# Kernel tuning notes

Measured on AMD Instinct MI355X. Metric: run time of the kernel, lower is better.

## Reference

```python
import jax, jax.numpy as jnp
import numpy as np

N_NODES = 100000
N_EDGES = 800000
IN_DIM = 7
HID = 64
HEADS1 = 4
NUM_CLUSTERS = 4
NEG_SLOPE = 0.2


def setup_inputs() -> dict:
    key = jax.random.key(0)
    ks = jax.random.split(key, 24)
    s = 0.1
    inp = {
        "x": jax.random.uniform(ks[0], (N_NODES, IN_DIM), dtype=jnp.float32),
        "edge_index": jax.random.randint(ks[1], (2, N_EDGES), 0, N_NODES, dtype=jnp.int32),
        "edge_attr": jax.random.normal(ks[2], (N_EDGES, 1), dtype=jnp.float32),
        "assignments": jax.random.randint(ks[3], (N_NODES,), 0, NUM_CLUSTERS, dtype=jnp.int32),
        "W1": jax.random.normal(ks[4], (IN_DIM, HEADS1 * HID), dtype=jnp.float32) * s,
        "att_src1": jax.random.normal(ks[5], (HEADS1, HID), dtype=jnp.float32) * s,
        "att_dst1": jax.random.normal(ks[6], (HEADS1, HID), dtype=jnp.float32) * s,
        "We1": jax.random.normal(ks[7], (1, HEADS1 * HID), dtype=jnp.float32) * s,
        "att_e1": jax.random.normal(ks[8], (HEADS1, HID), dtype=jnp.float32) * s,
        "b1": jnp.zeros((HEADS1 * HID,), dtype=jnp.float32),
        "W2": jax.random.normal(ks[9], (HEADS1 * HID, HID), dtype=jnp.float32) * s,
        "att_src2": jax.random.normal(ks[10], (1, HID), dtype=jnp.float32) * s,
        "att_dst2": jax.random.normal(ks[11], (1, HID), dtype=jnp.float32) * s,
        "We2": jax.random.normal(ks[12], (1, HID), dtype=jnp.float32) * s,
        "att_e2": jax.random.normal(ks[13], (1, HID), dtype=jnp.float32) * s,
        "b2": jnp.zeros((HID,), dtype=jnp.float32),
        # actor MLP: (HID+1) -> HID -> 1
        "A1": jax.random.normal(ks[14], (HID + 1, HID), dtype=jnp.float32) * s,
        "ba1": jnp.zeros((HID,), dtype=jnp.float32),
        "A2": jax.random.normal(ks[15], (HID, 1), dtype=jnp.float32) * s,
        "ba2": jnp.zeros((1,), dtype=jnp.float32),
        # critic MLP: HID*num_clusters -> HID -> 1
        "C1": jax.random.normal(ks[16], (HID * NUM_CLUSTERS, HID), dtype=jnp.float32) * s,
        "bc1": jnp.zeros((HID,), dtype=jnp.float32),
        "C2": jax.random.normal(ks[17], (HID, 1), dtype=jnp.float32) * s,
        "bc2": jnp.zeros((1,), dtype=jnp.float32),
    }
    return inp


def _segment_softmax(logits, seg, n):
    # logits: [E, H]; softmax over edges sharing the same dst node.
    m = jax.ops.segment_max(logits, seg, num_segments=n)
    e = jnp.exp(logits - m[seg])
    z = jax.ops.segment_sum(e, seg, num_segments=n)
    return e / z[seg]


def _gat_conv(x, edge_index, edge_attr, W, att_src, att_dst, We, att_e, bias,
              heads, out_dim, concat, n):
    src, dst = edge_index[0], edge_index[1]
    xh = (x @ W).reshape(n, heads, out_dim)                   # [N,H,D]
    a_src = (xh * att_src[None]).sum(-1)                      # [N,H]
    a_dst = (xh * att_dst[None]).sum(-1)                      # [N,H]
    eh = (edge_attr @ We).reshape(-1, heads, out_dim)         # [E,H,D]
    a_e = (eh * att_e[None]).sum(-1)                          # [E,H]
    alpha = jax.nn.leaky_relu(a_src[src] + a_dst[dst] + a_e, NEG_SLOPE)
    alpha = _segment_softmax(alpha, dst, n)                   # [E,H]
    msg = xh[src] * alpha[:, :, None]                         # [E,H,D]
    out = jax.ops.segment_sum(msg, dst, num_segments=n)       # [N,H,D]
    out = out.reshape(n, heads * out_dim) if concat else out.mean(axis=1)
    return out + bias


def reference(x, edge_index, edge_attr, assignments,
              W1, att_src1, att_dst1, We1, att_e1, b1,
              W2, att_src2, att_dst2, We2, att_e2, b2,
              A1, ba1, A2, ba2, C1, bc1, C2, bc2):
    n = x.shape[0]
    h = jax.nn.elu(_gat_conv(x, edge_index, edge_attr,
                             W1, att_src1, att_dst1, We1, att_e1, b1,
                             HEADS1, HID, True, n))
    h = _gat_conv(h, edge_index, edge_attr,
                  W2, att_src2, att_dst2, We2, att_e2, b2,
                  1, HID, False, n)                            # [N,HID]
    # cluster mean pooling (fused segment-reduce, replaces python loop)
    seg = assignments
    counts = jax.ops.segment_sum(jnp.ones((n,), dtype=h.dtype), seg,
                                 num_segments=NUM_CLUSTERS)
    denom = jnp.maximum(counts, 1.0)[:, None]
    z_clusters = jax.ops.segment_sum(h, seg, num_segments=NUM_CLUSTERS) / denom
    z_clusters = jnp.where(counts[:, None] > 0, z_clusters, 0.0)  # [C,HID]
    cf = jax.ops.segment_sum(x[:, 6], seg, num_segments=NUM_CLUSTERS) / denom[:, 0]
    cf = jnp.where(counts > 0, cf, 0.0)[:, None]                  # [C,1]
    z_with_cf = jnp.concatenate([z_clusters, cf], axis=-1)        # [C,HID+1]
    logits = (jax.nn.relu(z_with_cf @ A1 + ba1) @ A2 + ba2)[:, 0]  # [C]
    z_flat = z_clusters.reshape(1, -1)                             # [1,C*HID]
    value = jax.nn.relu(z_flat @ C1 + bc1) @ C2 + bc2              # [1,1]
    probs = jax.nn.softmax(logits)[None, :]                        # [1,C]
    return probs, value, z_flat
```

## Files before the change

kernel.cpp:

```cpp
#include <hip/hip_runtime.h>

#define NN 100000
#define NE 800000
#define NPB 512
#define SRCMASK 0x01FFFFFF

typedef short bf16x8 __attribute__((ext_vector_type(8)));
typedef float f32x4 __attribute__((ext_vector_type(4)));

__device__ __forceinline__ float wave_reduce_sum(float v) {
    #pragma unroll
    for (int o = 32; o > 0; o >>= 1) v += __shfl_down(v, o, 64);
    return v;
}

__device__ __forceinline__ unsigned short f2bf(float f) {
    unsigned u = __float_as_uint(f);
    unsigned r = (u + 0x7FFFu + ((u >> 16) & 1u)) >> 16;
    return (unsigned short)r;
}
__device__ __forceinline__ float bf2f(unsigned short b) {
    return __uint_as_float(((unsigned)b) << 16);
}
__device__ __forceinline__ float bflo(unsigned u) {
    return __uint_as_float(u << 16);
}
__device__ __forceinline__ float bfhi(unsigned u) {
    return __uint_as_float(u & 0xFFFF0000u);
}
__device__ __forceinline__ unsigned pk2(float a, float b) {
    return (unsigned)f2bf(a) | ((unsigned)f2bf(b) << 16);
}

__global__ void k_pre(const float* __restrict__ W1, const float* __restrict__ as1,
                      const float* __restrict__ ad1,
                      const float* __restrict__ We1, const float* __restrict__ ae1,
                      const float* __restrict__ We2, const float* __restrict__ ae2,
                      const float* __restrict__ W2, const float* __restrict__ as2,
                      const float* __restrict__ ad2,
                      float* __restrict__ cb, unsigned short* __restrict__ W2fr) {
    int t = threadIdx.x;
    if (blockIdx.x == 0) {
        if (t < 28) {
            int k = t >> 2, h = t & 3;
            float s = 0.f, d = 0.f;
            for (int c = 0; c < 64; ++c) {
                float w = W1[k * 256 + h * 64 + c];
                s += w * as1[h * 64 + c];
                d += w * ad1[h * 64 + c];
            }
            cb[t] = s; cb[28 + t] = d;
        } else if (t < 32) {
            int h = t - 28;
            float s = 0.f;
            for (int c = 0; c < 64; ++c) s += We1[h * 64 + c] * ae1[h * 64 + c];
            cb[56 + h] = s;
        } else if (t == 32) {
            float s = 0.f;
            for (int c = 0; c < 64; ++c) s += We2[c] * ae2[c];
            cb[60] = s;
        }
    } else {
        int o = (blockIdx.x - 1) * 256 + t;
        if (o >= 20480) return;
        int i = o & 7, l = (o >> 3) & 63, rest = o >> 9;
        int ct = rest % 5, ks = rest / 5;
        int k = ks * 32 + ((l >> 4) * 8) + i;
        int cl = l & 15;
        if (ct < 4) {
            W2fr[o] = f2bf(W2[k * 64 + ct * 16 + cl]);
        } else if (cl < 2) {
            const float* av = (cl == 0) ? as2 : ad2;
            float s = 0.f;
            for (int j = 0; j < 64; ++j) s += W2[k * 64 + j] * av[j];
            W2fr[o] = f2bf(s);
        } else {
            W2fr[o] = 0;
        }
    }
}

__global__ void k_node1h(const float* __restrict__ x, const float* __restrict__ cb,
                         const int* __restrict__ dst,
                         uint4* __restrict__ anode, uint4* __restrict__ xpack,
                         int* __restrict__ hist, int* __restrict__ rank) {
    int n = blockIdx.x * 256 + threadIdx.x;
    if (n >= NN) return;
    float xv[7];
    #pragma unroll
    for (int k = 0; k < 7; ++k) xv[k] = x[n * 7 + k];
    float s[4] = {0.f, 0.f, 0.f, 0.f}, d[4] = {0.f, 0.f, 0.f, 0.f};
    #pragma unroll
    for (int k = 0; k < 7; ++k)
        #pragma unroll
        for (int h = 0; h < 4; ++h) {
            s[h] += xv[k] * cb[k * 4 + h];
            d[h] += xv[k] * cb[28 + k * 4 + h];
        }
    anode[n] = make_uint4(pk2(s[0], s[1]), pk2(s[2], s[3]), pk2(d[0], d[1]), pk2(d[2], d[3]));
    xpack[n] = make_uint4(pk2(xv[0], xv[1]), pk2(xv[2], xv[3]),
                          pk2(xv[4], xv[5]), pk2(xv[6], 1.f));
    int e0 = n * 8;
    int4 d0 = *(const int4*)(dst + e0);
    int4 d1 = *(const int4*)(dst + e0 + 4);
    int4 r0, r1;
    r0.x = atomicAdd(&hist[d0.x], 1); r0.y = atomicAdd(&hist[d0.y], 1);
    r0.z = atomicAdd(&hist[d0.z], 1); r0.w = atomicAdd(&hist[d0.w], 1);
    r1.x = atomicAdd(&hist[d1.x], 1); r1.y = atomicAdd(&hist[d1.y], 1);
    r1.z = atomicAdd(&hist[d1.z], 1); r1.w = atomicAdd(&hist[d1.w], 1);
    *(int4*)(rank + e0) = r0;
    *(int4*)(rank + e0 + 4) = r1;
}

__global__ __launch_bounds__(1024) void k_scanA(const int* __restrict__ hist,
                                                int* __restrict__ bsum) {
    __shared__ int ws[16];
    int i = blockIdx.x * 1024 + threadIdx.x;
    int lane = threadIdx.x & 63, wid = threadIdx.x >> 6;
    int v = (i < NN) ? hist[i] : 0;
    #pragma unroll
    for (int o = 32; o; o >>= 1) v += __shfl_down(v, o, 64);
    if (lane == 0) ws[wid] = v;
    __syncthreads();
    if (wid == 0) {
        int u = (lane < 16) ? ws[lane] : 0;
        #pragma unroll
        for (int o = 8; o; o >>= 1) u += __shfl_down(u, o, 64);
        if (lane == 0) bsum[blockIdx.x] = u;
    }
}

__global__ void k_scanB(const int* __restrict__ bsum, int* __restrict__ bexcl) {
    __shared__ int w0tot;
    int t = threadIdx.x, lane = t & 63, wid = t >> 6;
    int v = (t < 98) ? bsum[t] : 0;
    int s = v;
    #pragma unroll
    for (int d = 1; d < 64; d <<= 1) { int u = __shfl_up(s, d, 64); if (lane >= d) s += u; }
    if (t == 63) w0tot = s;
    __syncthreads();
    if (wid == 1) s += w0tot;
    if (t < 98) bexcl[t] = s - v;
}

__global__ __launch_bounds__(1024) void k_scanC(const int* __restrict__ hist,
                                                const int* __restrict__ bexcl,
                                                int* __restrict__ offs) {
    __shared__ int ws[16];
    int b = blockIdx.x;
    int i = b * 1024 + threadIdx.x;
    int lane = threadIdx.x & 63, wid = threadIdx.x >> 6;
    int v = (i < NN) ? hist[i] : 0;
    int s = v;
    #pragma unroll
    for (int d = 1; d < 64; d <<= 1) { int u = __shfl_up(s, d, 64); if (lane >= d) s += u; }
    if (lane == 63) ws[wid] = s;
    __syncthreads();
    if (wid == 0) {
        int u2 = (lane < 16) ? ws[lane] : 0;
        #pragma unroll
        for (int d = 1; d < 16; d <<= 1) { int uu = __shfl_up(u2, d, 64); if (lane >= d) u2 += uu; }
        if (lane < 16) ws[lane] = u2;
    }
    __syncthreads();
    int incl = s + (wid ? ws[wid - 1] : 0) + bexcl[b];
    if (i < NN) offs[i + 1] = incl;
    if (i == 0) offs[0] = 0;
}

__global__ void k_scatter(const int* __restrict__ src, const int* __restrict__ dst,
                          const float* __restrict__ ea, const int* __restrict__ rank,
                          const int* __restrict__ offs,
                          const uint4* __restrict__ anode, const float* __restrict__ cb,
                          int4* __restrict__ es2) {
    int e0 = (blockIdx.x * 256 + threadIdx.x) * 2;
    if (e0 >= NE) return;
    int2 s2 = *(const int2*)(src + e0);
    int2 d2 = *(const int2*)(dst + e0);
    float2 a2 = *(const float2*)(ea + e0);
    int2 r2 = *(const int2*)(rank + e0);
    float c56 = cb[56], c57 = cb[57], c58 = cb[58], c59 = cb[59];
    #pragma unroll
    for (int u = 0; u < 2; ++u) {
        int s = u ? s2.y : s2.x;
        int d = u ? d2.y : d2.x;
        float eav = u ? a2.y : a2.x;
        int pos = offs[d] + (u ? r2.y : r2.x);
        uint4 ar = anode[s];
        uint4 br = anode[d];
        float lg0 = bflo(ar.x) + bflo(br.z) + eav * c56;
        float lg1 = bfhi(ar.x) + bfhi(br.z) + eav * c57;
        float lg2 = bflo(ar.y) + bflo(br.w) + eav * c58;
        float lg3 = bfhi(ar.y) + bfhi(br.w) + eav * c59;
        lg0 = lg0 >= 0.f ? lg0 : 0.2f * lg0;
        lg1 = lg1 >= 0.f ? lg1 : 0.2f * lg1;
        lg2 = lg2 >= 0.f ? lg2 : 0.2f * lg2;
        lg3 = lg3 >= 0.f ? lg3 : 0.2f * lg3;
        unsigned w01 = pk2(__expf(lg0), __expf(lg1));
        unsigned w23 = pk2(__expf(lg2), __expf(lg3));
        es2[pos] = make_int4((int)w01, (int)w23, s | ((d & 31) << 25), __float_as_int(eav));
    }
}

__global__ __launch_bounds__(256, 7) void k_conv1red(
    const uint4* __restrict__ xpack, const float* __restrict__ W1, const float* __restrict__ b1,
    const int* __restrict__ offs, const int4* __restrict__ es2,
    const unsigned short* __restrict__ W2fr,
    unsigned short* __restrict__ xh2b, float* __restrict__ a_src2, float* __restrict__ a_dst2) {
    __shared__ __attribute__((aligned(16))) unsigned char smem[16896];
    uint4* xs = (uint4*)smem;
    uint2* wsx = (uint2*)(smem + 4096);
    typedef unsigned short hsrow[264];
    hsrow* hs = (hsrow*)smem;
    __shared__ int soffs[33];
    __shared__ float ms[32][33];
    int t = threadIdx.x, lane = t & 63, wid = t >> 6;
    int n0 = blockIdx.x * 32;
    if (t <= 32) soffs[t] = offs[n0 + t];
    float w1r[7][4], b1r[4];
    #pragma unroll
    for (int k = 0; k < 7; ++k)
        #pragma unroll
        for (int h = 0; h < 4; ++h) w1r[k][h] = W1[k * 256 + h * 64 + lane];
    #pragma unroll
    for (int h = 0; h < 4; ++h) b1r[h] = b1[h * 64 + lane];
    __syncthreads();
    int E0 = soffs[0], E1 = soffs[32];
    int g = t >> 3, q = t & 7;
    int go0 = soffs[g], go1 = soffs[g + 1];
    int qh = q >> 1;
    int xsl = (q & 1) ? 0 : 16;
    float mh0 = 0.f, mh1 = 0.f, mh2 = 0.f, mh3 = 0.f;
    for (int C0 = E0; C0 < E1; C0 += 256) {
        int C1 = min(C0 + 256, E1);
        int j = C0 + t;
        if (j < C1) {
            int4 e4 = es2[j];
            xs[t] = xpack[e4.z & SRCMASK];
            wsx[t] = make_uint2((unsigned)e4.x, (unsigned)e4.y);
        }
        __syncthreads();
        int lo = max(go0, C0) - C0, hi = min(go1, C1) - C0;
        for (int jj = lo; jj < hi; ++jj) {
            unsigned xu = ((const unsigned*)&xs[jj])[qh];
            float xv = __uint_as_float((xu << xsl) & 0xFFFF0000u);
            uint2 wv = wsx[jj];
            mh0 = fmaf(bflo(wv.x), xv, mh0);
            mh1 = fmaf(bfhi(wv.x), xv, mh1);
            mh2 = fmaf(bflo(wv.y), xv, mh2);
            mh3 = fmaf(bfhi(wv.y), xv, mh3);
        }
        __syncthreads();
    }
    ms[g][0 * 8 + q] = mh0; ms[g][1 * 8 + q] = mh1;
    ms[g][2 * 8 + q] = mh2; ms[g][3 * 8 + q] = mh3;
    __syncthreads();
    for (int gi = wid * 8; gi < wid * 8 + 8; ++gi) {
        bool has = soffs[gi + 1] > soffs[gi];
        #pragma unroll
        for (int h = 0; h < 4; ++h) {
            float rz = __builtin_amdgcn_rcpf(ms[gi][h * 8 + 7]);
            float a = 0.f;
            #pragma unroll
            for (int k = 0; k < 7; ++k) a = fmaf(ms[gi][h * 8 + k], w1r[k][h], a);
            float mm = (has ? a * rz : 0.f) + b1r[h];
            float hv = mm > 0.f ? mm : (__expf(mm) - 1.f);
            hs[gi][h * 64 + lane] = f2bf(hv);
        }
    }
    __syncthreads();
    int row = lane & 15, kg = lane >> 4;
    #pragma unroll
    for (int u = wid; u < 10; u += 4) {
        int nt = u & 1, ct = u >> 1;
        f32x4 acc = {0.f, 0.f, 0.f, 0.f};
        #pragma unroll
        for (int ks = 0; ks < 8; ++ks) {
            bf16x8 av = *(const bf16x8*)&hs[nt * 16 + row][ks * 32 + kg * 8];
            bf16x8 bv = *(const bf16x8*)(W2fr + (((ks * 5 + ct) * 64) + lane) * 8);
            acc = __builtin_amdgcn_mfma_f32_16x16x32_bf16(av, bv, acc, 0, 0, 0);
        }
        if (ct < 4) {
            #pragma unroll
            for (int i = 0; i < 4; ++i)
                xh2b[(n0 + nt * 16 + kg * 4 + i) * 64 + ct * 16 + row] = f2bf(acc[i]);
        } else if (row == 0) {
            #pragma unroll
            for (int i = 0; i < 4; ++i) a_src2[n0 + nt * 16 + kg * 4 + i] = acc[i];
        } else if (row == 1) {
            #pragma unroll
            for (int i = 0; i < 4; ++i) a_dst2[n0 + nt * 16 + kg * 4 + i] = acc[i];
        }
    }
}

__global__ __launch_bounds__(256) void k_znorm(
    const int4* __restrict__ es2, const int* __restrict__ offs,
    const float* __restrict__ a_src2, const float* __restrict__ a_dst2,
    const int* __restrict__ assign, const float* __restrict__ cb,
    float* __restrict__ cs) {
    __shared__ int soffs[33];
    __shared__ float adL[32];
    __shared__ int asgL[32];
    __shared__ float ewL[512];
    __shared__ float rzL[32];
    __shared__ float zacc[32];
    int t = threadIdx.x;
    int n0 = blockIdx.x * 32;
    if (t <= 32) soffs[t] = offs[n0 + t];
    if (t < 32) { adL[t] = a_dst2[n0 + t]; asgL[t] = assign[n0 + t]; zacc[t] = 0.f; }
    __syncthreads();
    int E0 = soffs[0], E1 = soffs[32];
    float c2 = cb[60];
    int sx0 = 0, d50 = 0, sx1 = 0, d51 = 0;
    float ew0 = 0.f, ew1 = 0.f;
    bool h0 = (E0 + t) < E1, h1 = (E0 + 256 + t) < E1;
    if (h0) {
        int4 e4 = es2[E0 + t];
        sx0 = e4.z & SRCMASK; d50 = (e4.z >> 25) & 31;
        float lg = a_src2[sx0] + adL[d50] + __int_as_float(e4.w) * c2;
        lg = lg >= 0.f ? lg : 0.2f * lg;
        ew0 = __expf(lg);
        ewL[t] = ew0;
    }
    if (h1) {
        int4 e4 = es2[E0 + 256 + t];
        sx1 = e4.z & SRCMASK; d51 = (e4.z >> 25) & 31;
        float lg = a_src2[sx1] + adL[d51] + __int_as_float(e4.w) * c2;
        lg = lg >= 0.f ? lg : 0.2f * lg;
        ew1 = __expf(lg);
        ewL[256 + t] = ew1;
    }
    for (int j = E0 + 512 + t; j < E1; j += 256) {
        int4 e4 = es2[j];
        int d5 = (e4.z >> 25) & 31;
        float lg = a_src2[e4.z & SRCMASK] + adL[d5] + __int_as_float(e4.w) * c2;
        lg = lg >= 0.f ? lg : 0.2f * lg;
        atomicAdd(&zacc[d5], __expf(lg));
    }
    __syncthreads();
    int g = t >> 3, q = t & 7;
    int lo = soffs[g] - E0, hi = min(soffs[g + 1] - E0, 512);
    float z = 0.f;
    for (int jj = lo + q; jj < hi; jj += 8) z += ewL[jj];
    z += __shfl_xor(z, 1, 64);
    z += __shfl_xor(z, 2, 64);
    z += __shfl_xor(z, 4, 64);
    if (q == 0) rzL[g] = __builtin_amdgcn_rcpf(z + zacc[g]);
    __syncthreads();
    if (h0) atomicAdd(&cs[sx0 * 4 + asgL[d50]], ew0 * rzL[d50]);
    if (h1) atomicAdd(&cs[sx1 * 4 + asgL[d51]], ew1 * rzL[d51]);
    for (int j = E0 + 512 + t; j < E1; j += 256) {
        int4 e4 = es2[j];
        int sx = e4.z & SRCMASK, d5 = (e4.z >> 25) & 31;
        float lg = a_src2[sx] + adL[d5] + __int_as_float(e4.w) * c2;
        lg = lg >= 0.f ? lg : 0.2f * lg;
        atomicAdd(&cs[sx * 4 + asgL[d5]], __expf(lg) * rzL[d5]);
    }
}

__global__ __launch_bounds__(256) void k_pool(
    const unsigned short* __restrict__ xh2b, const float* __restrict__ cs,
    const int* __restrict__ assign, const float* __restrict__ x,
    float* __restrict__ gacc) {
    __shared__ float csum[264];
    int t = threadIdx.x;
    int q = t & 7, slot = t >> 3;
    float a0[8], a1[8], a2[8], a3[8];
    #pragma unroll
    for (int j = 0; j < 8; ++j) { a0[j] = 0.f; a1[j] = 0.f; a2[j] = 0.f; a3[j] = 0.f; }
    float cnt0 = 0.f, cnt1 = 0.f, cnt2 = 0.f, cnt3 = 0.f;
    float cf0 = 0.f, cf1 = 0.f, cf2 = 0.f, cf3 = 0.f;
    for (int n = blockIdx.x * 32 + slot; n < NN; n += NPB * 32) {
        uint4 u = *(const uint4*)(xh2b + n * 64 + q * 8);
        float4 c4 = *(const float4*)(cs + n * 4);
        float xv[8];
        xv[0] = bf2f((unsigned short)u.x); xv[1] = bf2f((unsigned short)(u.x >> 16));
        xv[2] = bf2f((unsigned short)u.y); xv[3] = bf2f((unsigned short)(u.y >> 16));
        xv[4] = bf2f((unsigned short)u.z); xv[5] = bf2f((unsigned short)(u.z >> 16));
        xv[6] = bf2f((unsigned short)u.w); xv[7] = bf2f((unsigned short)(u.w >> 16));
        #pragma unroll
        for (int j = 0; j < 8; ++j) {
            a0[j] = fmaf(c4.x, xv[j], a0[j]);
            a1[j] = fmaf(c4.y, xv[j], a1[j]);
            a2[j] = fmaf(c4.z, xv[j], a2[j]);
            a3[j] = fmaf(c4.w, xv[j], a3[j]);
        }
        if (q == 0) {
            int a = assign[n];
            float xf = x[n * 7 + 6];
            cnt0 += (a == 0) ? 1.f : 0.f;  cf0 += (a == 0) ? xf : 0.f;
            cnt1 += (a == 1) ? 1.f : 0.f;  cf1 += (a == 1) ? xf : 0.f;
            cnt2 += (a == 2) ? 1.f : 0.f;  cf2 += (a == 2) ? xf : 0.f;
            cnt3 += (a == 3) ? 1.f : 0.f;  cf3 += (a == 3) ? xf : 0.f;
        }
    }
    for (int i = t; i < 264; i += 256) csum[i] = 0.f;
    __syncthreads();
    int base = q * 8;
    #pragma unroll
    for (int j = 0; j < 8; ++j) {
        atomicAdd(&csum[0 * 64 + base + j], a0[j]);
        atomicAdd(&csum[1 * 64 + base + j], a1[j]);
        atomicAdd(&csum[2 * 64 + base + j], a2[j]);
        atomicAdd(&csum[3 * 64 + base + j], a3[j]);
    }
    if (q == 0) {
        atomicAdd(&csum[256], cnt0); atomicAdd(&csum[257], cnt1);
        atomicAdd(&csum[258], cnt2); atomicAdd(&csum[259], cnt3);
        atomicAdd(&csum[260], cf0);  atomicAdd(&csum[261], cf1);
        atomicAdd(&csum[262], cf2);  atomicAdd(&csum[263], cf3);
    }
    __syncthreads();
    for (int i = t; i < 264; i += 256) atomicAdd(&gacc[i], csum[i]);
}

__global__ __launch_bounds__(256) void k_head(
    const float* __restrict__ gacc, const float* __restrict__ b2,
    const float* __restrict__ A1, const float* __restrict__ ba1,
    const float* __restrict__ A2, const float* __restrict__ ba2,
    const float* __restrict__ C1, const float* __restrict__ bc1,
    const float* __restrict__ C2, const float* __restrict__ bc2,
    float* __restrict__ out) {
    __shared__ float zc[4][64];
    __shared__ float cfs[4];
    __shared__ float logits[4];
    __shared__ float vpart[4][64];
    int t = threadIdx.x;
    int j = t & 63, wv = t >> 6;
    float cnt = gacc[256 + wv];
    float den = fmaxf(cnt, 1.f);
    zc[wv][j] = (cnt > 0.f) ? (gacc[wv * 64 + j] + cnt * b2[j]) / den : 0.f;
    if (t < 4) {
        float cc = gacc[256 + t];
        cfs[t] = (cc > 0.f) ? gacc[260 + t] / fmaxf(cc, 1.f) : 0.f;
    }
    __syncthreads();
    float tv = ba1[j];
    for (int k = 0; k < 64; ++k) tv = fmaf(zc[wv][k], A1[k * 64 + j], tv);
    tv = fmaf(cfs[wv], A1[64 * 64 + j], tv);
    tv = fmaxf(tv, 0.f);
    float sred = wave_reduce_sum(tv * A2[j]);
    if (j == 0) logits[wv] = sred + ba2[0];
    float vj = (wv == 0) ? bc1[j] : 0.f;
    for (int kk = 0; kk < 64; ++kk) vj = fmaf(zc[wv][kk], C1[(wv * 64 + kk) * 64 + j], vj);
    vpart[wv][j] = vj;
    __syncthreads();
    if (wv == 0) {
        float vv = fmaxf(vpart[0][j] + vpart[1][j] + vpart[2][j] + vpart[3][j], 0.f);
        float v = wave_reduce_sum(vv * C2[j]);
        if (j == 0) {
            float m = fmaxf(fmaxf(logits[0], logits[1]), fmaxf(logits[2], logits[3]));
            float e0 = __expf(logits[0] - m), e1 = __expf(logits[1] - m);
            float e2 = __expf(logits[2] - m), e3 = __expf(logits[3] - m);
            float sum = e0 + e1 + e2 + e3;
            out[0] = e0 / sum; out[1] = e1 / sum; out[2] = e2 / sum; out[3] = e3 / sum;
            out[4] = v + bc2[0];
        }
    }
    out[5 + wv * 64 + j] = zc[wv][j];
}

extern "C" void kernel_launch(void* const* d_in, const int* in_sizes, int n_in,
                              void* d_out, int out_size, void* d_ws, size_t ws_size,
                              hipStream_t stream) {
    const float* x    = (const float*)d_in[0];
    const int*   ei   = (const int*)d_in[1];
    const float* ea   = (const float*)d_in[2];
    const int*   asg  = (const int*)d_in[3];
    const float* W1   = (const float*)d_in[4];
    const float* as1  = (const float*)d_in[5];
    const float* ad1  = (const float*)d_in[6];
    const float* We1  = (const float*)d_in[7];
    const float* ae1  = (const float*)d_in[8];
    const float* b1   = (const float*)d_in[9];
    const float* W2   = (const float*)d_in[10];
    const float* as2  = (const float*)d_in[11];
    const float* ad2  = (const float*)d_in[12];
    const float* We2  = (const float*)d_in[13];
    const float* ae2  = (const float*)d_in[14];
    const float* b2   = (const float*)d_in[15];
    const float* A1   = (const float*)d_in[16];
    const float* ba1  = (const float*)d_in[17];
    const float* A2   = (const float*)d_in[18];
    const float* ba2  = (const float*)d_in[19];
    const float* C1   = (const float*)d_in[20];
    const float* bc1  = (const float*)d_in[21];
    const float* C2   = (const float*)d_in[22];
    const float* bc2  = (const float*)d_in[23];
    const int* src = ei;
    const int* dst = ei + NE;

    char* w = (char*)d_ws;
    size_t off = 0;
    auto alloc = [&](size_t bytes) -> void* {
        void* p = w + off;
        off += (bytes + 255) & ~(size_t)255;
        return p;
    };
    int*   hist   = (int*)alloc(NN * sizeof(int));
    float* cs     = (float*)alloc(NN * 4 * sizeof(float));
    float* gacc   = (float*)alloc(264 * sizeof(float));
    size_t zspan  = (size_t)((char*)gacc + 264 * sizeof(float) - (char*)hist);
    uint4* anode  = (uint4*)alloc(NN * sizeof(uint4));
    float* a_src2 = (float*)alloc(NN * sizeof(float));
    float* a_dst2 = (float*)alloc(NN * sizeof(float));
    uint4* xpack  = (uint4*)alloc(NN * sizeof(uint4));
    int*   offs   = (int*)alloc((NN + 1) * sizeof(int));
    int*   rank   = (int*)alloc(NE * sizeof(int));
    int*   bsum   = (int*)alloc(128 * sizeof(int));
    int*   bexcl  = (int*)alloc(128 * sizeof(int));
    int4*  es2    = (int4*)alloc(NE * sizeof(int4));
    unsigned short* xh2b = (unsigned short*)alloc(NN * 64 * sizeof(unsigned short));
    unsigned short* W2fr = (unsigned short*)alloc(20480 * sizeof(unsigned short));
    float* cb     = (float*)alloc(64 * sizeof(float));
    (void)ws_size; (void)n_in; (void)in_sizes; (void)out_size;

    (void)hipMemsetAsync(hist, 0, zspan, stream);

    k_pre<<<81, 256, 0, stream>>>(W1, as1, ad1, We1, ae1, We2, ae2, W2, as2, ad2, cb, W2fr);
    k_node1h<<<(NN + 255) / 256, 256, 0, stream>>>(x, cb, dst, anode, xpack, hist, rank);
    k_scanA<<<98, 1024, 0, stream>>>(hist, bsum);
    k_scanB<<<1, 128, 0, stream>>>(bsum, bexcl);
    k_scanC<<<98, 1024, 0, stream>>>(hist, bexcl, offs);
    k_scatter<<<(NE / 2 + 255) / 256, 256, 0, stream>>>(src, dst, ea, rank, offs,
                                                        anode, cb, es2);
    k_conv1red<<<NN / 32, 256, 0, stream>>>(xpack, W1, b1, offs, es2,
                                            W2fr, xh2b, a_src2, a_dst2);
    k_znorm<<<NN / 32, 256, 0, stream>>>(es2, offs, a_src2, a_dst2, asg, cb, cs);
    k_pool<<<NPB, 256, 0, stream>>>(xh2b, cs, asg, x, gacc);
    k_head<<<1, 256, 0, stream>>>(gacc, b2, A1, ba1, A2, ba2, C1, bc1, C2, bc2, (float*)d_out);
}
```

Before: 192.3 us.

## Fuse conv2 softmax normalization with cluster pooling via dst-side gather

Replaces the scatter of normalized attention weights into a per-source cluster-weight array and the later pooling pass. Each dst-node group now gathers source features (bf16 rows) weighted by the normalized attention and accumulates them into its cluster. Per-block partial sums are written out and reduced by a new deterministic reduce kernel instead of global atomics. This removes 800K global float atomics and the NN×4 intermediate plus its memset. In exchange it adds a gather of 128-byte rows per edge, which means more memory traffic (about 100MB versus roughly 13MB for the node-side pass), and only 8 threads are active per destination node.

```diff
diff --git a/kernel.cpp b/kernel.cpp
--- a/kernel.cpp
+++ b/kernel.cpp
@@ -2,7 +2,7 @@
 
 #define NN 100000
 #define NE 800000
-#define NPB 512
+#define NZB (NN / 32)
 #define SRCMASK 0x01FFFFFF
 
 typedef short bf16x8 __attribute__((ext_vector_type(8)));
@@ -294,42 +294,45 @@
     }
 }
 
-__global__ __launch_bounds__(256) void k_znorm(
+__global__ __launch_bounds__(256) void k_zpool(
     const int4* __restrict__ es2, const int* __restrict__ offs,
     const float* __restrict__ a_src2, const float* __restrict__ a_dst2,
     const int* __restrict__ assign, const float* __restrict__ cb,
-    float* __restrict__ cs) {
+    const unsigned short* __restrict__ xh2b, const float* __restrict__ x,
+    float* __restrict__ partial) {
     __shared__ int soffs[33];
     __shared__ float adL[32];
     __shared__ int asgL[32];
     __shared__ float ewL[512];
+    __shared__ int sL[512];
     __shared__ float rzL[32];
     __shared__ float zacc[32];
+    __shared__ float csum[264];
     int t = threadIdx.x;
     int n0 = blockIdx.x * 32;
     if (t <= 32) soffs[t] = offs[n0 + t];
     if (t < 32) { adL[t] = a_dst2[n0 + t]; asgL[t] = assign[n0 + t]; zacc[t] = 0.f; }
+    for (int i = t; i < 264; i += 256) csum[i] = 0.f;
     __syncthreads();
     int E0 = soffs[0], E1 = soffs[32];
     float c2 = cb[60];
-    int sx0 = 0, d50 = 0, sx1 = 0, d51 = 0;
-    float ew0 = 0.f, ew1 = 0.f;
-    bool h0 = (E0 + t) < E1, h1 = (E0 + 256 + t) < E1;
-    if (h0) {
+    if (E0 + t < E1) {
         int4 e4 = es2[E0 + t];
-        sx0 = e4.z & SRCMASK; d50 = (e4.z >> 25) & 31;
-        float lg = a_src2[sx0] + adL[d50] + __int_as_float(e4.w) * c2;
+        int sx = e4.z & SRCMASK;
+        int d5 = (e4.z >> 25) & 31;
+        float lg = a_src2[sx] + adL[d5] + __int_as_float(e4.w) * c2;
         lg = lg >= 0.f ? lg : 0.2f * lg;
-        ew0 = __expf(lg);
-        ewL[t] = ew0;
-    }
-    if (h1) {
+        ewL[t] = __expf(lg);
+        sL[t] = sx;
+    }
+    if (E0 + 256 + t < E1) {
         int4 e4 = es2[E0 + 256 + t];
-        sx1 = e4.z & SRCMASK; d51 = (e4.z >> 25) & 31;
-        float lg = a_src2[sx1] + adL[d51] + __int_as_float(e4.w) * c2;
+        int sx = e4.z & SRCMASK;
+        int d5 = (e4.z >> 25) & 31;
+        float lg = a_src2[sx] + adL[d5] + __int_as_float(e4.w) * c2;
         lg = lg >= 0.f ? lg : 0.2f * lg;
-        ew1 = __expf(lg);
-        ewL[256 + t] = ew1;
+        ewL[256 + t] = __expf(lg);
+        sL[256 + t] = sx;
     }
     for (int j = E0 + 512 + t; j < E1; j += 256) {
         int4 e4 = es2[j];
@@ -340,79 +343,59 @@
     }
     __syncthreads();
     int g = t >> 3, q = t & 7;
-    int lo = soffs[g] - E0, hi = min(soffs[g + 1] - E0, 512);
+    int lo = soffs[g] - E0, hi = soffs[g + 1] - E0;
+    int hicap = min(hi, 512);
     float z = 0.f;
-    for (int jj = lo + q; jj < hi; jj += 8) z += ewL[jj];
+    for (int jj = lo + q; jj < hicap; jj += 8) z += ewL[jj];
     z += __shfl_xor(z, 1, 64);
     z += __shfl_xor(z, 2, 64);
     z += __shfl_xor(z, 4, 64);
     if (q == 0) rzL[g] = __builtin_amdgcn_rcpf(z + zacc[g]);
     __syncthreads();
-    if (h0) atomicAdd(&cs[sx0 * 4 + asgL[d50]], ew0 * rzL[d50]);
-    if (h1) atomicAdd(&cs[sx1 * 4 + asgL[d51]], ew1 * rzL[d51]);
-    for (int j = E0 + 512 + t; j < E1; j += 256) {
-        int4 e4 = es2[j];
-        int sx = e4.z & SRCMASK, d5 = (e4.z >> 25) & 31;
-        float lg = a_src2[sx] + adL[d5] + __int_as_float(e4.w) * c2;
+    float rzv = rzL[g];
+    float a0 = 0.f, a1 = 0.f, a2 = 0.f, a3 = 0.f;
+    float a4 = 0.f, a5 = 0.f, a6 = 0.f, a7 = 0.f;
+    for (int jj = lo; jj < hicap; ++jj) {
+        float wv = ewL[jj] * rzv;
+        int sj = sL[jj];
+        uint4 u = *(const uint4*)(xh2b + sj * 64 + q * 8);
+        a0 = fmaf(wv, bflo(u.x), a0); a1 = fmaf(wv, bfhi(u.x), a1);
+        a2 = fmaf(wv, bflo(u.y), a2); a3 = fmaf(wv, bfhi(u.y), a3);
+        a4 = fmaf(wv, bflo(u.z), a4); a5 = fmaf(wv, bfhi(u.z), a5);
+        a6 = fmaf(wv, bflo(u.w), a6); a7 = fmaf(wv, bfhi(u.w), a7);
+    }
+    for (int jo = max(lo, 512); jo < hi; ++jo) {
+        int4 e4 = es2[E0 + jo];
+        int sx = e4.z & SRCMASK;
+        float lg = a_src2[sx] + adL[g] + __int_as_float(e4.w) * c2;
         lg = lg >= 0.f ? lg : 0.2f * lg;
-        atomicAdd(&cs[sx * 4 + asgL[d5]], __expf(lg) * rzL[d5]);
-    }
-}
-
-__global__ __launch_bounds__(256) void k_pool(
-    const unsigned short* __restrict__ xh2b, const float* __restrict__ cs,
-    const int* __restrict__ assign, const float* __restrict__ x,
-    float* __restrict__ gacc) {
-    __shared__ float csum[264];
-    int t = threadIdx.x;
-    int q = t & 7, slot = t >> 3;
-    float a0[8], a1[8], a2[8], a3[8];
-    #pragma unroll
-    for (int j = 0; j < 8; ++j) { a0[j] = 0.f; a1[j] = 0.f; a2[j] = 0.f; a3[j] = 0.f; }
-    float cnt0 = 0.f, cnt1 = 0.f, cnt2 = 0.f, cnt3 = 0.f;
-    float cf0 = 0.f, cf1 = 0.f, cf2 = 0.f, cf3 = 0.f;
-    for (int n = blockIdx.x * 32 + slot; n < NN; n += NPB * 32) {
-        uint4 u = *(const uint4*)(xh2b + n * 64 + q * 8);
-        float4 c4 = *(const float4*)(cs + n * 4);
-        float xv[8];
-        xv[0] = bf2f((unsigned short)u.x); xv[1] = bf2f((unsigned short)(u.x >> 16));
-        xv[2] = bf2f((unsigned short)u.y); xv[3] = bf2f((unsigned short)(u.y >> 16));
-        xv[4] = bf2f((unsigned short)u.z); xv[5] = bf2f((unsigned short)(u.z >> 16));
-        xv[6] = bf2f((unsigned short)u.w); xv[7] = bf2f((unsigned short)(u.w >> 16));
-        #pragma unroll
-        for (int j = 0; j < 8; ++j) {
-            a0[j] = fmaf(c4.x, xv[j], a0[j]);
-            a1[j] = fmaf(c4.y, xv[j], a1[j]);
-            a2[j] = fmaf(c4.z, xv[j], a2[j]);
-            a3[j] = fmaf(c4.w, xv[j], a3[j]);
-        }
-        if (q == 0) {
-            int a = assign[n];
-            float xf = x[n * 7 + 6];
-            cnt0 += (a == 0) ? 1.f : 0.f;  cf0 += (a == 0) ? xf : 0.f;
-            cnt1 += (a == 1) ? 1.f : 0.f;  cf1 += (a == 1) ? xf : 0.f;
-            cnt2 += (a == 2) ? 1.f : 0.f;  cf2 += (a == 2) ? xf : 0.f;
-            cnt3 += (a == 3) ? 1.f : 0.f;  cf3 += (a == 3) ? xf : 0.f;
-        }
-    }
-    for (int i = t; i < 264; i += 256) csum[i] = 0.f;
-    __syncthreads();
-    int base = q * 8;
-    #pragma unroll
-    for (int j = 0; j < 8; ++j) {
-        atomicAdd(&csum[0 * 64 + base + j], a0[j]);
-        atomicAdd(&csum[1 * 64 + base + j], a1[j]);
-        atomicAdd(&csum[2 * 64 + base + j], a2[j]);
-        atomicAdd(&csum[3 * 64 + base + j], a3[j]);
-    }
-    if (q == 0) {
-        atomicAdd(&csum[256], cnt0); atomicAdd(&csum[257], cnt1);
-        atomicAdd(&csum[258], cnt2); atomicAdd(&csum[259], cnt3);
-        atomicAdd(&csum[260], cf0);  atomicAdd(&csum[261], cf1);
-        atomicAdd(&csum[262], cf2);  atomicAdd(&csum[263], cf3);
-    }
-    __syncthreads();
-    for (int i = t; i < 264; i += 256) atomicAdd(&gacc[i], csum[i]);
+        float wv = __expf(lg) * rzv;
+        uint4 u = *(const uint4*)(xh2b + sx * 64 + q * 8);
+        a0 = fmaf(wv, bflo(u.x), a0); a1 = fmaf(wv, bfhi(u.x), a1);
+        a2 = fmaf(wv, bflo(u.y), a2); a3 = fmaf(wv, bfhi(u.y), a3);
+        a4 = fmaf(wv, bflo(u.z), a4); a5 = fmaf(wv, bfhi(u.z), a5);
+        a6 = fmaf(wv, bflo(u.w), a6); a7 = fmaf(wv, bfhi(u.w), a7);
+    }
+    int cb_ = asgL[g] * 64 + q * 8;
+    atomicAdd(&csum[cb_ + 0], a0); atomicAdd(&csum[cb_ + 1], a1);
+    atomicAdd(&csum[cb_ + 2], a2); atomicAdd(&csum[cb_ + 3], a3);
+    atomicAdd(&csum[cb_ + 4], a4); atomicAdd(&csum[cb_ + 5], a5);
+    atomicAdd(&csum[cb_ + 6], a6); atomicAdd(&csum[cb_ + 7], a7);
+    if (t < 32) {
+        int c = asgL[t];
+        atomicAdd(&csum[256 + c], 1.f);
+        atomicAdd(&csum[260 + c], x[(n0 + t) * 7 + 6]);
+    }
+    __syncthreads();
+    for (int i = t; i < 264; i += 256) partial[blockIdx.x * 264 + i] = csum[i];
+}
+
+__global__ void k_red(const float* __restrict__ partial, float* __restrict__ gacc) {
+    int i = blockIdx.x;
+    float s = 0.f;
+    for (int b = threadIdx.x; b < NZB; b += 64) s += partial[b * 264 + i];
+    s = wave_reduce_sum(s);
+    if (threadIdx.x == 0) gacc[i] = s;
 }
 
 __global__ __launch_bounds__(256) void k_head(
@@ -499,9 +482,8 @@
         return p;
     };
     int*   hist   = (int*)alloc(NN * sizeof(int));
-    float* cs     = (float*)alloc(NN * 4 * sizeof(float));
     float* gacc   = (float*)alloc(264 * sizeof(float));
-    size_t zspan  = (size_t)((char*)gacc + 264 * sizeof(float) - (char*)hist);
+    float* partial= (float*)alloc((size_t)NZB * 264 * sizeof(float));
     uint4* anode  = (uint4*)alloc(NN * sizeof(uint4));
     float* a_src2 = (float*)alloc(NN * sizeof(float));
     float* a_dst2 = (float*)alloc(NN * sizeof(float));
@@ -516,7 +498,7 @@
     float* cb     = (float*)alloc(64 * sizeof(float));
     (void)ws_size; (void)n_in; (void)in_sizes; (void)out_size;
 
-    (void)hipMemsetAsync(hist, 0, zspan, stream);
+    (void)hipMemsetAsync(hist, 0, NN * sizeof(int), stream);
 
     k_pre<<<81, 256, 0, stream>>>(W1, as1, ad1, We1, ae1, We2, ae2, W2, as2, ad2, cb, W2fr);
     k_node1h<<<(NN + 255) / 256, 256, 0, stream>>>(x, cb, dst, anode, xpack, hist, rank);
@@ -527,7 +509,7 @@
                                                         anode, cb, es2);
     k_conv1red<<<NN / 32, 256, 0, stream>>>(xpack, W1, b1, offs, es2,
                                             W2fr, xh2b, a_src2, a_dst2);
-    k_znorm<<<NN / 32, 256, 0, stream>>>(es2, offs, a_src2, a_dst2, asg, cb, cs);
-    k_pool<<<NPB, 256, 0, stream>>>(xh2b, cs, asg, x, gacc);
+    k_zpool<<<NZB, 256, 0, stream>>>(es2, offs, a_src2, a_dst2, asg, cb, xh2b, x, partial);
+    k_red<<<264, 64, 0, stream>>>(partial, gacc);
     k_head<<<1, 256, 0, stream>>>(gacc, b2, A1, ba1, A2, ba2, C1, bc1, C2, bc2, (float*)d_out);
 }
```

Measured after the change: 187.0 us. 2.8% less time.
